# Performance work log

Hardware: AMD Instinct MI355X
Metric: run time of the kernel (lower is better)

## Reference

```python
import jax, jax.numpy as jnp
import numpy as np

B, S, HID = 1, 4096, 1024
HQ, HKV, D = 16, 4, 64   # query heads, kv heads (GQA), dim_per_head
ROPE_BASE = 10000.0


def setup_inputs() -> dict:
    key = jax.random.key(0)
    ks = jax.random.split(key, 5)
    s = 0.02
    return {
        "x": jax.random.normal(ks[0], (B, S, HID), jnp.float32),
        "Wq": jax.random.normal(ks[1], (HID, HQ * D), jnp.float32) * s,
        "Wk": jax.random.normal(ks[2], (HID, HKV * D), jnp.float32) * s,
        "Wv": jax.random.normal(ks[3], (HID, HKV * D), jnp.float32) * s,
        "Wo": jax.random.normal(ks[4], (HQ * D, HID), jnp.float32) * s,
    }


def _rope(t, cos, sin):
    # non-interleaved (half-split) rotary; t: [B,S,H,D], cos/sin: [S, D//2]
    t1, t2 = jnp.split(t, 2, axis=-1)
    c = cos[None, :, None, :]
    sn = sin[None, :, None, :]
    return jnp.concatenate([t1 * c - t2 * sn, t2 * c + t1 * sn], axis=-1)


def reference(x, Wq, Wk, Wv, Wo):
    # QKV projections (self-attention: key=value=query=x), reshape to [B,S,H,D]
    q = (x @ Wq).reshape(B, S, HQ, D)
    k = (x @ Wk).reshape(B, S, HKV, D)
    v = (x @ Wv).reshape(B, S, HKV, D)

    # rotary position embedding over full head dim
    inv_freq = 1.0 / (ROPE_BASE ** (jnp.arange(0, D, 2, dtype=jnp.float32) / D))
    ang = jnp.arange(S, dtype=jnp.float32)[:, None] * inv_freq[None, :]  # [S, D//2]
    cos, sin = jnp.cos(ang), jnp.sin(ang)
    q = _rope(q, cos, sin)
    k = _rope(k, cos, sin)

    # GQA: expand kv heads to match query heads
    g = HQ // HKV
    k = jnp.repeat(k, g, axis=2)
    v = jnp.repeat(v, g, axis=2)

    scale = D ** -0.5  # attn_scaling ** -0.5 with attn_scaling = dim_per_head
    scores = jnp.einsum('bqhd,bkhd->bhqk', q, k) * scale  # [B,HQ,S,S]
    causal = jnp.tril(jnp.ones((S, S), dtype=bool))
    scores = jnp.where(causal[None, None], scores, jnp.finfo(scores.dtype).min)
    attn = jax.nn.softmax(scores, axis=-1)

    ctx = jnp.einsum('bhqk,bkhd->bqhd', attn, v).reshape(B, S, HQ * D)
    return ctx @ Wo
```

## Files before the change

kernel.cpp:

```cpp
#include <hip/hip_runtime.h>
#include <hip/hip_bf16.h>
#include <math.h>

typedef __attribute__((ext_vector_type(8))) short short8;
typedef __attribute__((ext_vector_type(4))) float f32x4;

#define S_   4096
#define HQ_  16
#define HKV_ 4
#define D_   64

static __device__ __forceinline__ unsigned short f2b(float f) {
    __hip_bfloat16 h = __float2bfloat16(f);
    return *reinterpret_cast<unsigned short*>(&h);
}
static __device__ __forceinline__ float b2f(unsigned short u) {
    union { unsigned int u; float f; } c;
    c.u = ((unsigned int)u) << 16;
    return c.f;
}

typedef __attribute__((address_space(1))) const unsigned int gas_u32;
typedef __attribute__((address_space(3))) unsigned int las_u32;
static __device__ __forceinline__ void gload16(const void* g, void* l) {
    __builtin_amdgcn_global_load_lds((gas_u32*)g, (las_u32*)l, 16, 0, 0);
}


__global__ __launch_bounds__(256) void k_prep(const float* __restrict__ Wq,
                                              const float* __restrict__ Wk,
                                              const float* __restrict__ Wv,
                                              const float* __restrict__ Wo,
                                              const float* __restrict__ x,
                                              unsigned short* __restrict__ WT,
                                              unsigned short* __restrict__ WoT,
                                              unsigned short* __restrict__ xb,
                                              float* __restrict__ cs) {
    const int z = blockIdx.z;
    const int t = threadIdx.x;
    if (z == 4) {
        int flat = blockIdx.y * 32 + blockIdx.x;
#pragma unroll
        for (int ii = 0; ii < 4; ++ii) {
            int i = flat * 1024 + ii * 256 + t;
            float4 v = ((const float4*)x)[i];
            ushort4 o;
            o.x = f2b(v.x); o.y = f2b(v.y); o.z = f2b(v.z); o.w = f2b(v.w);
            ((ushort4*)xb)[i] = o;
        }
        return;
    }
    if (z == 5) {
        int flat = blockIdx.y * 32 + blockIdx.x;
        if (flat >= 512) return;
        int i = flat * 256 + t;
        int s = i >> 5, jj = i & 31;
        float invf = exp2f(-(float)jj * (13.287712379549449f / 32.0f));
        float ang = (float)s * invf;
        ((float2*)cs)[i] = make_float2(cosf(ang), sinf(ang));
        return;
    }
    const float* tin; unsigned short* tout; int N, gx;
    if (z == 0)      { tin = Wq; tout = WT;                 N = 1024; gx = 32; }
    else if (z == 1) { tin = Wk; tout = WT + 1024 * 1024;   N = 256;  gx = 8;  }
    else if (z == 2) { tin = Wv; tout = WT + 1280 * 1024;   N = 256;  gx = 8;  }
    else             { tin = Wo; tout = WoT;                N = 1024; gx = 32; }
    if ((int)blockIdx.x >= gx) return;
    __shared__ float tile[32][33];
    int tx = t & 31, ty = t >> 5;
    int n0 = blockIdx.x * 32, k0 = blockIdx.y * 32;
#pragma unroll
    for (int r = 0; r < 32; r += 8)
        tile[ty + r][tx] = tin[(size_t)(k0 + ty + r) * N + n0 + tx];
    __syncthreads();
#pragma unroll
    for (int r = 0; r < 32; r += 8)
        tout[(size_t)(n0 + ty + r) * 1024 + k0 + tx] = f2b(tile[tx][ty + r]);
}


__global__ __launch_bounds__(256) void k_gemm_qkv(const unsigned short* __restrict__ A,
                                                  const unsigned short* __restrict__ BT,
                                                  const float* __restrict__ cs,
                                                  unsigned short* __restrict__ Qr,
                                                  unsigned short* __restrict__ Kr,
                                                  unsigned short* __restrict__ Vt) {
    __shared__ unsigned short As[128 * 64];
    __shared__ unsigned short Bs[64 * 64];
    const int t = threadIdx.x;
    const int ntile = blockIdx.x;
    const int n0 = ntile * 64;
    const int m0 = blockIdx.y * 128;
    const int w = t >> 6, lane = t & 63, lr = lane & 15, lg = lane >> 4;
    const int sr = lane >> 3, sch = (lane & 7) * 16;
    const int K = 1024;

    f32x4 acc[2][4];
#pragma unroll
    for (int m = 0; m < 2; ++m)
#pragma unroll
        for (int n = 0; n < 4; ++n) acc[m][n] = (f32x4){0.f, 0.f, 0.f, 0.f};

    for (int k0 = 0; k0 < K; k0 += 64) {
#pragma unroll
        for (int c = 0; c < 4; ++c) {
            int r0 = w * 32 + c * 8;
            int r = r0 + sr;
            gload16((const char*)&A[(size_t)(m0 + r) * K + k0] + (sch ^ ((r & 7) << 4)),
                    (char*)As + r0 * 128);
        }
#pragma unroll
        for (int c = 0; c < 2; ++c) {
            int r0 = w * 16 + c * 8;
            int r = r0 + sr;
            gload16((const char*)&BT[(size_t)(n0 + r) * K + k0] + (sch ^ ((r & 7) << 4)),
                    (char*)Bs + r0 * 128);
        }
        __syncthreads();
#pragma unroll
        for (int kk = 0; kk < 2; ++kk) {
            short8 af[2], bf[4];
#pragma unroll
            for (int m = 0; m < 2; ++m) {
                int arow = w * 32 + m * 16 + lr;
                af[m] = *(const short8*)((const char*)As + arow * 128 +
                                         ((kk * 64 + lg * 16) ^ ((arow & 7) << 4)));
            }
#pragma unroll
            for (int n = 0; n < 4; ++n) {
                int brow = n * 16 + lr;
                bf[n] = *(const short8*)((const char*)Bs + brow * 128 +
                                         ((kk * 64 + lg * 16) ^ ((brow & 7) << 4)));
            }
#pragma unroll
            for (int m = 0; m < 2; ++m)
#pragma unroll
                for (int n = 0; n < 4; ++n)
                    acc[m][n] = __builtin_amdgcn_mfma_f32_16x16x32_bf16(af[m], bf[n], acc[m][n], 0, 0, 0);
        }
        __syncthreads();
    }

    if (ntile < 20) {
        const float QS = (ntile < 16) ? 0.125f * 1.44269504088896340736f : 1.0f;
        unsigned short* dst = (ntile < 16) ? (Qr + (size_t)ntile * (S_ * D_))
                                           : (Kr + (size_t)(ntile - 16) * (S_ * D_));
#pragma unroll
        for (int m = 0; m < 2; ++m)
#pragma unroll
            for (int rr = 0; rr < 4; ++rr) {
                int s = m0 + w * 32 + m * 16 + lg * 4 + rr;
                const float2* csr = (const float2*)cs + s * 32;
                float2 c0 = csr[lr];
                float2 c1 = csr[16 + lr];
                float t1 = acc[m][0][rr], t2 = acc[m][2][rr];
                dst[(size_t)s * 64 + lr]      = f2b((t1 * c0.x - t2 * c0.y) * QS);
                dst[(size_t)s * 64 + 32 + lr] = f2b((t2 * c0.x + t1 * c0.y) * QS);
                t1 = acc[m][1][rr]; t2 = acc[m][3][rr];
                dst[(size_t)s * 64 + 16 + lr] = f2b((t1 * c1.x - t2 * c1.y) * QS);
                dst[(size_t)s * 64 + 48 + lr] = f2b((t2 * c1.x + t1 * c1.y) * QS);
            }
    } else {
        int h2 = ntile - 20;
        unsigned short* dst = Vt + (size_t)h2 * (D_ * S_);
#pragma unroll
        for (int m = 0; m < 2; ++m)
#pragma unroll
            for (int n = 0; n < 4; ++n)
#pragma unroll
                for (int rr = 0; rr < 4; ++rr) {
                    int s = m0 + w * 32 + m * 16 + lg * 4 + rr;
                    dst[(size_t)(n * 16 + lr) * S_ + s] = f2b(acc[m][n][rr]);
                }
    }
}


__global__ __launch_bounds__(256) void k_gemm_o(const unsigned short* __restrict__ A,
                                                const unsigned short* __restrict__ BT,
                                                float* __restrict__ out) {
    __shared__ unsigned short As[128 * 64];
    __shared__ unsigned short Bs[64 * 64];
    const int t = threadIdx.x;
    const int n0 = blockIdx.x * 64;
    const int m0 = blockIdx.y * 128;
    const int w = t >> 6, lane = t & 63, lr = lane & 15, lg = lane >> 4;
    const int sr = lane >> 3, sch = (lane & 7) * 16;
    const int K = 1024;

    f32x4 acc[2][4];
#pragma unroll
    for (int m = 0; m < 2; ++m)
#pragma unroll
        for (int n = 0; n < 4; ++n) acc[m][n] = (f32x4){0.f, 0.f, 0.f, 0.f};

    for (int k0 = 0; k0 < K; k0 += 64) {
#pragma unroll
        for (int c = 0; c < 4; ++c) {
            int r0 = w * 32 + c * 8;
            int r = r0 + sr;
            gload16((const char*)&A[(size_t)(m0 + r) * K + k0] + (sch ^ ((r & 7) << 4)),
                    (char*)As + r0 * 128);
        }
#pragma unroll
        for (int c = 0; c < 2; ++c) {
            int r0 = w * 16 + c * 8;
            int r = r0 + sr;
            gload16((const char*)&BT[(size_t)(n0 + r) * K + k0] + (sch ^ ((r & 7) << 4)),
                    (char*)Bs + r0 * 128);
        }
        __syncthreads();
#pragma unroll
        for (int kk = 0; kk < 2; ++kk) {
            short8 af[2], bf[4];
#pragma unroll
            for (int m = 0; m < 2; ++m) {
                int arow = w * 32 + m * 16 + lr;
                af[m] = *(const short8*)((const char*)As + arow * 128 +
                                         ((kk * 64 + lg * 16) ^ ((arow & 7) << 4)));
            }
#pragma unroll
            for (int n = 0; n < 4; ++n) {
                int brow = n * 16 + lr;
                bf[n] = *(const short8*)((const char*)Bs + brow * 128 +
                                         ((kk * 64 + lg * 16) ^ ((brow & 7) << 4)));
            }
#pragma unroll
            for (int m = 0; m < 2; ++m)
#pragma unroll
                for (int n = 0; n < 4; ++n)
                    acc[m][n] = __builtin_amdgcn_mfma_f32_16x16x32_bf16(af[m], bf[n], acc[m][n], 0, 0, 0);
        }
        __syncthreads();
    }
#pragma unroll
    for (int m = 0; m < 2; ++m)
#pragma unroll
        for (int n = 0; n < 4; ++n)
#pragma unroll
            for (int rr = 0; rr < 4; ++rr) {
                int row = m0 + w * 32 + m * 16 + lg * 4 + rr;
                int col = n0 + n * 16 + lr;
                out[(size_t)row * 1024 + col] = acc[m][n][rr];
            }
}


__global__ __launch_bounds__(256, 2)
void k_attn(const unsigned short* __restrict__ Qr,
            const unsigned short* __restrict__ Kr,
            const unsigned short* __restrict__ Vt,
            unsigned short* __restrict__ Pacc,
            float* __restrict__ Psv) {
    __shared__ unsigned short Ks[2][64 * 64];
    __shared__ unsigned short Vs[2][64 * 64];
    __shared__ unsigned short Ps[4][32 * 64];

    const int t = threadIdx.x;
    const int p = blockIdx.x;
    const int h = blockIdx.y;
    const int j = blockIdx.z;
    const int kvh = h >> 2;
    const int w = t >> 6, lane = t & 63, lr = lane & 15, lg = lane >> 4;

    const unsigned short* Qh = Qr + (size_t)h * (S_ * D_);
    const unsigned short* Kh = Kr + (size_t)kvh * (S_ * D_);
    const unsigned short* Vh = Vt + (size_t)kvh * (D_ * S_);

    const int xw = (lr & 7) << 4;
    const int sr = lane >> 3, sch = (lane & 7) * 16;
    const int r0a = w * 16, r0b = w * 16 + 8;

#pragma unroll 1
    for (int half = 0; half < 2; ++half) {
        const int qb = half ? p : (31 - p);
        const int lastkb = 2 * qb + 1;
        const int qi0 = qb * 128 + w * 32 + lr;

        const char* kp[2];
        const char* vp[2];
        {
            int ra = r0a + sr, rb = r0b + sr;
            kp[0] = (const char*)(Kh + (size_t)(j * 64 + ra) * 64) + (sch ^ ((ra & 7) << 4));
            kp[1] = (const char*)(Kh + (size_t)(j * 64 + rb) * 64) + (sch ^ ((rb & 7) << 4));
            vp[0] = (const char*)(Vh + (size_t)ra * S_ + j * 64) + (sch ^ ((ra & 7) << 4));
            vp[1] = (const char*)(Vh + (size_t)rb * S_ + j * 64) + (sch ^ ((rb & 7) << 4));
        }
        auto stage = [&](int buf) {
            gload16(kp[0], (char*)&Ks[buf][0] + r0a * 128);
            gload16(kp[1], (char*)&Ks[buf][0] + r0b * 128);
            gload16(vp[0], (char*)&Vs[buf][0] + r0a * 128);
            gload16(vp[1], (char*)&Vs[buf][0] + r0b * 128);
            kp[0] += 16384; kp[1] += 16384;
            vp[0] += 256;   vp[1] += 256;
        };

        short8 aq[2][2];
        {
            int q0 = (qb * 128 + w * 32 + lr);
            aq[0][0] = *(const short8*)&Qh[(size_t)q0 * 64 + lg * 8];
            aq[0][1] = *(const short8*)&Qh[(size_t)q0 * 64 + 32 + lg * 8];
            aq[1][0] = *(const short8*)&Qh[(size_t)(q0 + 16) * 64 + lg * 8];
            aq[1][1] = *(const short8*)&Qh[(size_t)(q0 + 16) * 64 + 32 + lg * 8];
        }
        float svl0 = 0.f, svl1 = 0.f;
        f32x4 acc0[4], acc1[4];
#pragma unroll
        for (int i = 0; i < 4; ++i) { acc0[i] = (f32x4){0.f,0.f,0.f,0.f}; acc1[i] = (f32x4){0.f,0.f,0.f,0.f}; }

        int cur = 0;
        stage(0);
        __syncthreads();

        for (int kb = j; kb <= lastkb; kb += 2) {
            if (kb + 2 <= lastkb) stage(cur ^ 1);

            f32x4 s0[4], s1[4];
#pragma unroll
            for (int i = 0; i < 4; ++i) { s0[i] = (f32x4){0.f,0.f,0.f,0.f}; s1[i] = (f32x4){0.f,0.f,0.f,0.f}; }
            const char* KsB = (const char*)&Ks[cur][0];
            __builtin_amdgcn_s_setprio(1);
#pragma unroll
            for (int kk = 0; kk < 2; ++kk)
#pragma unroll
                for (int nt = 0; nt < 4; ++nt) {
                    int brow = nt * 16 + lr;
                    short8 kf = *(const short8*)(KsB + brow * 128 + ((kk * 64 + lg * 16) ^ xw));
                    s0[nt] = __builtin_amdgcn_mfma_f32_16x16x32_bf16(kf, aq[0][kk], s0[nt], 0, 0, 0);
                    s1[nt] = __builtin_amdgcn_mfma_f32_16x16x32_bf16(kf, aq[1][kk], s1[nt], 0, 0, 0);
                }
            __builtin_amdgcn_s_setprio(0);

            if (kb >= 2 * qb) {
                int kbase = kb * 64 + lg * 4;
#pragma unroll
                for (int nt = 0; nt < 4; ++nt)
#pragma unroll
                    for (int rr = 0; rr < 4; ++rr) {
                        int ki = kbase + nt * 16 + rr;
                        if (ki > qi0) s0[nt][rr] = -INFINITY;
                        if (ki > qi0 + 16) s1[nt][rr] = -INFINITY;
                    }
            }

            char* PwB = (char*)&Ps[w][0];
#pragma unroll
            for (int nt = 0; nt < 4; ++nt) {
                float p0 = exp2f(s0[nt][0]), p1 = exp2f(s0[nt][1]);
                float p2 = exp2f(s0[nt][2]), p3 = exp2f(s0[nt][3]);
                svl0 += (p0 + p1) + (p2 + p3);
                unsigned int w0, w1;
                asm("v_cvt_pk_bf16_f32 %0, %1, %2" : "=v"(w0) : "v"(p0), "v"(p1));
                asm("v_cvt_pk_bf16_f32 %0, %1, %2" : "=v"(w1) : "v"(p2), "v"(p3));
                union { unsigned int u32[2]; unsigned long long u64; } pk;
                pk.u32[0] = w0; pk.u32[1] = w1;
                *(unsigned long long*)(PwB + lr * 128 + ((nt * 32 + lg * 8) ^ xw)) = pk.u64;
            }
#pragma unroll
            for (int nt = 0; nt < 4; ++nt) {
                float p0 = exp2f(s1[nt][0]), p1 = exp2f(s1[nt][1]);
                float p2 = exp2f(s1[nt][2]), p3 = exp2f(s1[nt][3]);
                svl1 += (p0 + p1) + (p2 + p3);
                unsigned int w0, w1;
                asm("v_cvt_pk_bf16_f32 %0, %1, %2" : "=v"(w0) : "v"(p0), "v"(p1));
                asm("v_cvt_pk_bf16_f32 %0, %1, %2" : "=v"(w1) : "v"(p2), "v"(p3));
                union { unsigned int u32[2]; unsigned long long u64; } pk;
                pk.u32[0] = w0; pk.u32[1] = w1;
                *(unsigned long long*)(PwB + (16 + lr) * 128 + ((nt * 32 + lg * 8) ^ xw)) = pk.u64;
            }

            const char* VsB = (const char*)&Vs[cur][0];
            __builtin_amdgcn_s_setprio(1);
#pragma unroll
            for (int kk = 0; kk < 2; ++kk) {
                short8 pa0 = *(const short8*)(PwB + lr * 128 + ((kk * 64 + lg * 16) ^ xw));
                short8 pa1 = *(const short8*)(PwB + (16 + lr) * 128 + ((kk * 64 + lg * 16) ^ xw));
#pragma unroll
                for (int nt = 0; nt < 4; ++nt) {
                    int drow = nt * 16 + lr;
                    short8 vb = *(const short8*)(VsB + drow * 128 + ((kk * 64 + lg * 16) ^ xw));
                    acc0[nt] = __builtin_amdgcn_mfma_f32_16x16x32_bf16(pa0, vb, acc0[nt], 0, 0, 0);
                    acc1[nt] = __builtin_amdgcn_mfma_f32_16x16x32_bf16(pa1, vb, acc1[nt], 0, 0, 0);
                }
            }
            __builtin_amdgcn_s_setprio(0);

            __syncthreads();
            cur ^= 1;
        }

        svl0 += __shfl_xor(svl0, 16); svl0 += __shfl_xor(svl0, 32);
        svl1 += __shfl_xor(svl1, 16); svl1 += __shfl_xor(svl1, 32);
        const int u = (j * 32 + qb) * 16 + h;
        if (lg == 0) {
            Psv[u * 128 + w * 32 + lr] = svl0;
            Psv[u * 128 + w * 32 + 16 + lr] = svl1;
        }
        unsigned short* Pb = Pacc + (size_t)u * 8192;
#pragma unroll
        for (int nt = 0; nt < 4; ++nt)
#pragma unroll
            for (int rr = 0; rr < 4; ++rr) {
                int row0 = w * 32 + lg * 4 + rr;
                int col = nt * 16 + lr;
                Pb[row0 * 64 + col] = f2b(acc0[nt][rr]);
                Pb[(row0 + 16) * 64 + col] = f2b(acc1[nt][rr]);
            }
    }
}


__global__ __launch_bounds__(256) void k_combine(const unsigned short* __restrict__ Pacc,
                                                 const float* __restrict__ Psv,
                                                 unsigned short* __restrict__ O) {
    const int qb64 = blockIdx.x, h = blockIdx.y;
    const int t = threadIdx.x;
    const int r = t >> 2, db = (t & 3) * 16;
    const int qb128 = qb64 >> 1;
    const int rloc = (qb64 & 1) * 64 + r;
    const int u0 = qb128 * 16 + h;
    const int u1 = (32 + qb128) * 16 + h;
    float sa = Psv[u0 * 128 + rloc], sb = Psv[u1 * 128 + rloc];
    float inv = 1.f / (sa + sb);
    const unsigned short* A_ = Pacc + (size_t)u0 * 8192 + rloc * 64 + db;
    const unsigned short* B_ = Pacc + (size_t)u1 * 8192 + rloc * 64 + db;
    unsigned short* Op = O + (size_t)(qb64 * 64 + r) * 1024 + h * 64 + db;
#pragma unroll
    for (int halfv = 0; halfv < 2; ++halfv) {
        short8 va = *(const short8*)(A_ + halfv * 8);
        short8 vb = *(const short8*)(B_ + halfv * 8);
        short8 o;
#pragma unroll
        for (int i = 0; i < 8; ++i)
            o[i] = (short)f2b((b2f((unsigned short)va[i]) + b2f((unsigned short)vb[i])) * inv);
        *(short8*)(Op + halfv * 8) = o;
    }
}


extern "C" void kernel_launch(void* const* d_in, const int* in_sizes, int n_in,
                              void* d_out, int out_size, void* d_ws, size_t ws_size,
                              hipStream_t stream) {
    const float* x  = (const float*)d_in[0];
    const float* Wq = (const float*)d_in[1];
    const float* Wk = (const float*)d_in[2];
    const float* Wv = (const float*)d_in[3];
    const float* Wo = (const float*)d_in[4];
    float* out = (float*)d_out;
    char* ws = (char*)d_ws;

    unsigned short* WT  = (unsigned short*)(ws + 0);
    unsigned short* WoT = (unsigned short*)(ws + 3145728);
    unsigned short* Qr  = (unsigned short*)(ws + 5242880);
    unsigned short* Kr  = (unsigned short*)(ws + 13631488);
    unsigned short* Vt  = (unsigned short*)(ws + 15728640);
    unsigned short* O   = (unsigned short*)(ws + 17825792);
    float* cs           = (float*)(ws + 26214400);
    unsigned short* xb  = (unsigned short*)(ws + 27262976);
    unsigned short* Pacc = (unsigned short*)(ws + 27262976);
    float* Psv           = (float*)(ws + 44040192);

    k_prep<<<dim3(32, 32, 6), 256, 0, stream>>>(Wq, Wk, Wv, Wo, x, WT, WoT, xb, cs);
    k_gemm_qkv<<<dim3(24, 32), 256, 0, stream>>>(xb, WT, cs, Qr, Kr, Vt);
    k_attn<<<dim3(16, 16, 2), 256, 0, stream>>>(Qr, Kr, Vt, Pacc, Psv);
    k_combine<<<dim3(64, 16), 256, 0, stream>>>(Pacc, Psv, O);
    k_gemm_o<<<dim3(16, 32), 256, 0, stream>>>(O, WoT, out);
}
```

Measured before the change: 115.8 us.

## Halve attention query tile, keep P in registers, deepen GEMM K-step

The attention kernel now gives each wave 16 query rows (64-row blocks, twice as many blocks) and passes the softmax probabilities from the score MFMA output straight into the PV MFMA operand in registers. This removes the per-wave shared-memory P buffer and its write/read round trip. The V fragment load is split into two 8-byte loads to match the resulting register layout. Both GEMMs stage 128-wide K tiles per barrier instead of 64, with an occupancy hint of 3, which halves loop iterations and synchronisations at the cost of more LDS per block.

```diff
diff --git a/kernel.cpp b/kernel.cpp
--- a/kernel.cpp
+++ b/kernel.cpp
@@ -79,20 +79,22 @@
 }
 
 
-__global__ __launch_bounds__(256) void k_gemm_qkv(const unsigned short* __restrict__ A,
-                                                  const unsigned short* __restrict__ BT,
-                                                  const float* __restrict__ cs,
-                                                  unsigned short* __restrict__ Qr,
-                                                  unsigned short* __restrict__ Kr,
-                                                  unsigned short* __restrict__ Vt) {
-    __shared__ unsigned short As[128 * 64];
-    __shared__ unsigned short Bs[64 * 64];
+__global__ __launch_bounds__(256, 3)
+void k_gemm_qkv(const unsigned short* __restrict__ A,
+                const unsigned short* __restrict__ BT,
+                const float* __restrict__ cs,
+                unsigned short* __restrict__ Qr,
+                unsigned short* __restrict__ Kr,
+                unsigned short* __restrict__ Vt) {
+    __shared__ unsigned short As[128 * 128];
+    __shared__ unsigned short Bs[64 * 128];
     const int t = threadIdx.x;
     const int ntile = blockIdx.x;
     const int n0 = ntile * 64;
     const int m0 = blockIdx.y * 128;
     const int w = t >> 6, lane = t & 63, lr = lane & 15, lg = lane >> 4;
-    const int sr = lane >> 3, sch = (lane & 7) * 16;
+    const int srr = w * 4 + (lane >> 4);
+    const int sby = (lane & 15) * 16;
     const int K = 1024;
 
     f32x4 acc[2][4];
@@ -101,35 +103,33 @@
 #pragma unroll
         for (int n = 0; n < 4; ++n) acc[m][n] = (f32x4){0.f, 0.f, 0.f, 0.f};
 
-    for (int k0 = 0; k0 < K; k0 += 64) {
+    for (int k0 = 0; k0 < K; k0 += 128) {
+#pragma unroll
+        for (int c = 0; c < 8; ++c) {
+            int r = c * 16 + srr;
+            gload16((const char*)&A[(size_t)(m0 + r) * K + k0] + (sby ^ ((r & 7) << 4)),
+                    (char*)As + c * 4096 + w * 1024);
+        }
 #pragma unroll
         for (int c = 0; c < 4; ++c) {
-            int r0 = w * 32 + c * 8;
-            int r = r0 + sr;
-            gload16((const char*)&A[(size_t)(m0 + r) * K + k0] + (sch ^ ((r & 7) << 4)),
-                    (char*)As + r0 * 128);
-        }
-#pragma unroll
-        for (int c = 0; c < 2; ++c) {
-            int r0 = w * 16 + c * 8;
-            int r = r0 + sr;
-            gload16((const char*)&BT[(size_t)(n0 + r) * K + k0] + (sch ^ ((r & 7) << 4)),
-                    (char*)Bs + r0 * 128);
+            int r = c * 16 + srr;
+            gload16((const char*)&BT[(size_t)(n0 + r) * K + k0] + (sby ^ ((r & 7) << 4)),
+                    (char*)Bs + c * 4096 + w * 1024);
         }
         __syncthreads();
 #pragma unroll
-        for (int kk = 0; kk < 2; ++kk) {
+        for (int kk = 0; kk < 4; ++kk) {
             short8 af[2], bf[4];
 #pragma unroll
             for (int m = 0; m < 2; ++m) {
                 int arow = w * 32 + m * 16 + lr;
-                af[m] = *(const short8*)((const char*)As + arow * 128 +
+                af[m] = *(const short8*)((const char*)As + arow * 256 +
                                          ((kk * 64 + lg * 16) ^ ((arow & 7) << 4)));
             }
 #pragma unroll
             for (int n = 0; n < 4; ++n) {
                 int brow = n * 16 + lr;
-                bf[n] = *(const short8*)((const char*)Bs + brow * 128 +
+                bf[n] = *(const short8*)((const char*)Bs + brow * 256 +
                                          ((kk * 64 + lg * 16) ^ ((brow & 7) << 4)));
             }
 #pragma unroll
@@ -176,16 +176,18 @@
 }
 
 
-__global__ __launch_bounds__(256) void k_gemm_o(const unsigned short* __restrict__ A,
-                                                const unsigned short* __restrict__ BT,
-                                                float* __restrict__ out) {
-    __shared__ unsigned short As[128 * 64];
-    __shared__ unsigned short Bs[64 * 64];
+__global__ __launch_bounds__(256, 3)
+void k_gemm_o(const unsigned short* __restrict__ A,
+              const unsigned short* __restrict__ BT,
+              float* __restrict__ out) {
+    __shared__ unsigned short As[128 * 128];
+    __shared__ unsigned short Bs[64 * 128];
     const int t = threadIdx.x;
     const int n0 = blockIdx.x * 64;
     const int m0 = blockIdx.y * 128;
     const int w = t >> 6, lane = t & 63, lr = lane & 15, lg = lane >> 4;
-    const int sr = lane >> 3, sch = (lane & 7) * 16;
+    const int srr = w * 4 + (lane >> 4);
+    const int sby = (lane & 15) * 16;
     const int K = 1024;
 
     f32x4 acc[2][4];
@@ -194,35 +196,33 @@
 #pragma unroll
         for (int n = 0; n < 4; ++n) acc[m][n] = (f32x4){0.f, 0.f, 0.f, 0.f};
 
-    for (int k0 = 0; k0 < K; k0 += 64) {
+    for (int k0 = 0; k0 < K; k0 += 128) {
+#pragma unroll
+        for (int c = 0; c < 8; ++c) {
+            int r = c * 16 + srr;
+            gload16((const char*)&A[(size_t)(m0 + r) * K + k0] + (sby ^ ((r & 7) << 4)),
+                    (char*)As + c * 4096 + w * 1024);
+        }
 #pragma unroll
         for (int c = 0; c < 4; ++c) {
-            int r0 = w * 32 + c * 8;
-            int r = r0 + sr;
-            gload16((const char*)&A[(size_t)(m0 + r) * K + k0] + (sch ^ ((r & 7) << 4)),
-                    (char*)As + r0 * 128);
-        }
-#pragma unroll
-        for (int c = 0; c < 2; ++c) {
-            int r0 = w * 16 + c * 8;
-            int r = r0 + sr;
-            gload16((const char*)&BT[(size_t)(n0 + r) * K + k0] + (sch ^ ((r & 7) << 4)),
-                    (char*)Bs + r0 * 128);
+            int r = c * 16 + srr;
+            gload16((const char*)&BT[(size_t)(n0 + r) * K + k0] + (sby ^ ((r & 7) << 4)),
+                    (char*)Bs + c * 4096 + w * 1024);
         }
         __syncthreads();
 #pragma unroll
-        for (int kk = 0; kk < 2; ++kk) {
+        for (int kk = 0; kk < 4; ++kk) {
             short8 af[2], bf[4];
 #pragma unroll
             for (int m = 0; m < 2; ++m) {
                 int arow = w * 32 + m * 16 + lr;
-                af[m] = *(const short8*)((const char*)As + arow * 128 +
+                af[m] = *(const short8*)((const char*)As + arow * 256 +
                                          ((kk * 64 + lg * 16) ^ ((arow & 7) << 4)));
             }
 #pragma unroll
             for (int n = 0; n < 4; ++n) {
                 int brow = n * 16 + lr;
-                bf[n] = *(const short8*)((const char*)Bs + brow * 128 +
+                bf[n] = *(const short8*)((const char*)Bs + brow * 256 +
                                          ((kk * 64 + lg * 16) ^ ((brow & 7) << 4)));
             }
 #pragma unroll
@@ -246,7 +246,7 @@
 }
 
 
-__global__ __launch_bounds__(256, 2)
+__global__ __launch_bounds__(256, 4)
 void k_attn(const unsigned short* __restrict__ Qr,
             const unsigned short* __restrict__ Kr,
             const unsigned short* __restrict__ Vt,
@@ -254,7 +254,6 @@
             float* __restrict__ Psv) {
     __shared__ unsigned short Ks[2][64 * 64];
     __shared__ unsigned short Vs[2][64 * 64];
-    __shared__ unsigned short Ps[4][32 * 64];
 
     const int t = threadIdx.x;
     const int p = blockIdx.x;
@@ -273,9 +272,9 @@
 
 #pragma unroll 1
     for (int half = 0; half < 2; ++half) {
-        const int qb = half ? p : (31 - p);
-        const int lastkb = 2 * qb + 1;
-        const int qi0 = qb * 128 + w * 32 + lr;
+        const int qb = half ? p : (63 - p);
+        const int tend = qb + 1;
+        const int qi = qb * 64 + w * 16 + lr;
 
         const char* kp[2];
         const char* vp[2];
@@ -295,29 +294,27 @@
             vp[0] += 256;   vp[1] += 256;
         };
 
-        short8 aq[2][2];
+        short8 aq[2];
         {
-            int q0 = (qb * 128 + w * 32 + lr);
-            aq[0][0] = *(const short8*)&Qh[(size_t)q0 * 64 + lg * 8];
-            aq[0][1] = *(const short8*)&Qh[(size_t)q0 * 64 + 32 + lg * 8];
-            aq[1][0] = *(const short8*)&Qh[(size_t)(q0 + 16) * 64 + lg * 8];
-            aq[1][1] = *(const short8*)&Qh[(size_t)(q0 + 16) * 64 + 32 + lg * 8];
-        }
-        float svl0 = 0.f, svl1 = 0.f;
-        f32x4 acc0[4], acc1[4];
-#pragma unroll
-        for (int i = 0; i < 4; ++i) { acc0[i] = (f32x4){0.f,0.f,0.f,0.f}; acc1[i] = (f32x4){0.f,0.f,0.f,0.f}; }
+            int qrow = qb * 64 + w * 16 + lr;
+            aq[0] = *(const short8*)&Qh[(size_t)qrow * 64 + lg * 8];
+            aq[1] = *(const short8*)&Qh[(size_t)qrow * 64 + 32 + lg * 8];
+        }
+        float svl = 0.f;
+        f32x4 acc_o[4];
+#pragma unroll
+        for (int i = 0; i < 4; ++i) acc_o[i] = (f32x4){0.f, 0.f, 0.f, 0.f};
 
         int cur = 0;
         stage(0);
         __syncthreads();
 
-        for (int kb = j; kb <= lastkb; kb += 2) {
-            if (kb + 2 <= lastkb) stage(cur ^ 1);
-
-            f32x4 s0[4], s1[4];
-#pragma unroll
-            for (int i = 0; i < 4; ++i) { s0[i] = (f32x4){0.f,0.f,0.f,0.f}; s1[i] = (f32x4){0.f,0.f,0.f,0.f}; }
+        for (int kb = j; kb < tend; kb += 2) {
+            if (kb + 2 < tend) stage(cur ^ 1);
+
+            f32x4 s[4];
+#pragma unroll
+            for (int i = 0; i < 4; ++i) s[i] = (f32x4){0.f, 0.f, 0.f, 0.f};
             const char* KsB = (const char*)&Ks[cur][0];
             __builtin_amdgcn_s_setprio(1);
 #pragma unroll
@@ -326,61 +323,45 @@
                 for (int nt = 0; nt < 4; ++nt) {
                     int brow = nt * 16 + lr;
                     short8 kf = *(const short8*)(KsB + brow * 128 + ((kk * 64 + lg * 16) ^ xw));
-                    s0[nt] = __builtin_amdgcn_mfma_f32_16x16x32_bf16(kf, aq[0][kk], s0[nt], 0, 0, 0);
-                    s1[nt] = __builtin_amdgcn_mfma_f32_16x16x32_bf16(kf, aq[1][kk], s1[nt], 0, 0, 0);
+                    s[nt] = __builtin_amdgcn_mfma_f32_16x16x32_bf16(kf, aq[kk], s[nt], 0, 0, 0);
                 }
             __builtin_amdgcn_s_setprio(0);
 
-            if (kb >= 2 * qb) {
+            if (kb == qb) {
                 int kbase = kb * 64 + lg * 4;
 #pragma unroll
                 for (int nt = 0; nt < 4; ++nt)
 #pragma unroll
-                    for (int rr = 0; rr < 4; ++rr) {
-                        int ki = kbase + nt * 16 + rr;
-                        if (ki > qi0) s0[nt][rr] = -INFINITY;
-                        if (ki > qi0 + 16) s1[nt][rr] = -INFINITY;
-                    }
-            }
-
-            char* PwB = (char*)&Ps[w][0];
+                    for (int rr = 0; rr < 4; ++rr)
+                        if (kbase + nt * 16 + rr > qi) s[nt][rr] = -INFINITY;
+            }
+
+            unsigned int wd[8];
 #pragma unroll
             for (int nt = 0; nt < 4; ++nt) {
-                float p0 = exp2f(s0[nt][0]), p1 = exp2f(s0[nt][1]);
-                float p2 = exp2f(s0[nt][2]), p3 = exp2f(s0[nt][3]);
-                svl0 += (p0 + p1) + (p2 + p3);
-                unsigned int w0, w1;
-                asm("v_cvt_pk_bf16_f32 %0, %1, %2" : "=v"(w0) : "v"(p0), "v"(p1));
-                asm("v_cvt_pk_bf16_f32 %0, %1, %2" : "=v"(w1) : "v"(p2), "v"(p3));
-                union { unsigned int u32[2]; unsigned long long u64; } pk;
-                pk.u32[0] = w0; pk.u32[1] = w1;
-                *(unsigned long long*)(PwB + lr * 128 + ((nt * 32 + lg * 8) ^ xw)) = pk.u64;
-            }
-#pragma unroll
-            for (int nt = 0; nt < 4; ++nt) {
-                float p0 = exp2f(s1[nt][0]), p1 = exp2f(s1[nt][1]);
-                float p2 = exp2f(s1[nt][2]), p3 = exp2f(s1[nt][3]);
-                svl1 += (p0 + p1) + (p2 + p3);
-                unsigned int w0, w1;
-                asm("v_cvt_pk_bf16_f32 %0, %1, %2" : "=v"(w0) : "v"(p0), "v"(p1));
-                asm("v_cvt_pk_bf16_f32 %0, %1, %2" : "=v"(w1) : "v"(p2), "v"(p3));
-                union { unsigned int u32[2]; unsigned long long u64; } pk;
-                pk.u32[0] = w0; pk.u32[1] = w1;
-                *(unsigned long long*)(PwB + (16 + lr) * 128 + ((nt * 32 + lg * 8) ^ xw)) = pk.u64;
+                float p0 = exp2f(s[nt][0]), p1 = exp2f(s[nt][1]);
+                float p2 = exp2f(s[nt][2]), p3 = exp2f(s[nt][3]);
+                svl += (p0 + p1) + (p2 + p3);
+                asm("v_cvt_pk_bf16_f32 %0, %1, %2" : "=v"(wd[nt * 2])     : "v"(p0), "v"(p1));
+                asm("v_cvt_pk_bf16_f32 %0, %1, %2" : "=v"(wd[nt * 2 + 1]) : "v"(p2), "v"(p3));
             }
 
             const char* VsB = (const char*)&Vs[cur][0];
             __builtin_amdgcn_s_setprio(1);
 #pragma unroll
             for (int kk = 0; kk < 2; ++kk) {
-                short8 pa0 = *(const short8*)(PwB + lr * 128 + ((kk * 64 + lg * 16) ^ xw));
-                short8 pa1 = *(const short8*)(PwB + (16 + lr) * 128 + ((kk * 64 + lg * 16) ^ xw));
+                union { unsigned int u[4]; short8 s8; } pa;
+                pa.u[0] = wd[4 * kk + 0]; pa.u[1] = wd[4 * kk + 1];
+                pa.u[2] = wd[4 * kk + 2]; pa.u[3] = wd[4 * kk + 3];
 #pragma unroll
                 for (int nt = 0; nt < 4; ++nt) {
                     int drow = nt * 16 + lr;
-                    short8 vb = *(const short8*)(VsB + drow * 128 + ((kk * 64 + lg * 16) ^ xw));
-                    acc0[nt] = __builtin_amdgcn_mfma_f32_16x16x32_bf16(pa0, vb, acc0[nt], 0, 0, 0);
-                    acc1[nt] = __builtin_amdgcn_mfma_f32_16x16x32_bf16(pa1, vb, acc1[nt], 0, 0, 0);
+                    union { unsigned long long q[2]; short8 s8; } vb;
+                    vb.q[0] = *(const unsigned long long*)(VsB + drow * 128 +
+                              ((kk * 64 + lg * 8) ^ xw));
+                    vb.q[1] = *(const unsigned long long*)(VsB + drow * 128 +
+                              ((kk * 64 + 32 + lg * 8) ^ xw));
+                    acc_o[nt] = __builtin_amdgcn_mfma_f32_16x16x32_bf16(pa.s8, vb.s8, acc_o[nt], 0, 0, 0);
                 }
             }
             __builtin_amdgcn_s_setprio(0);
@@ -389,23 +370,20 @@
             cur ^= 1;
         }
 
-        svl0 += __shfl_xor(svl0, 16); svl0 += __shfl_xor(svl0, 32);
-        svl1 += __shfl_xor(svl1, 16); svl1 += __shfl_xor(svl1, 32);
-        const int u = (j * 32 + qb) * 16 + h;
-        if (lg == 0) {
-            Psv[u * 128 + w * 32 + lr] = svl0;
-            Psv[u * 128 + w * 32 + 16 + lr] = svl1;
-        }
-        unsigned short* Pb = Pacc + (size_t)u * 8192;
-#pragma unroll
-        for (int nt = 0; nt < 4; ++nt)
-#pragma unroll
-            for (int rr = 0; rr < 4; ++rr) {
-                int row0 = w * 32 + lg * 4 + rr;
-                int col = nt * 16 + lr;
-                Pb[row0 * 64 + col] = f2b(acc0[nt][rr]);
-                Pb[(row0 + 16) * 64 + col] = f2b(acc1[nt][rr]);
-            }
+        svl += __shfl_xor(svl, 16);
+        svl += __shfl_xor(svl, 32);
+        const int u = ((j * 64 + qb) * 16 + h);
+        if (lg == 0) Psv[u * 64 + w * 16 + lr] = svl;
+        unsigned short* Pb = Pacc + (size_t)u * 4096;
+#pragma unroll
+        for (int nt = 0; nt < 4; ++nt) {
+            int rr = w * 16 + lg * 4;
+            int col = nt * 16 + lr;
+            Pb[(rr + 0) * 64 + col] = f2b(acc_o[nt][0]);
+            Pb[(rr + 1) * 64 + col] = f2b(acc_o[nt][1]);
+            Pb[(rr + 2) * 64 + col] = f2b(acc_o[nt][2]);
+            Pb[(rr + 3) * 64 + col] = f2b(acc_o[nt][3]);
+        }
     }
 }
 
@@ -413,18 +391,16 @@
 __global__ __launch_bounds__(256) void k_combine(const unsigned short* __restrict__ Pacc,
                                                  const float* __restrict__ Psv,
                                                  unsigned short* __restrict__ O) {
-    const int qb64 = blockIdx.x, h = blockIdx.y;
+    const int qb = blockIdx.x, h = blockIdx.y;
     const int t = threadIdx.x;
     const int r = t >> 2, db = (t & 3) * 16;
-    const int qb128 = qb64 >> 1;
-    const int rloc = (qb64 & 1) * 64 + r;
-    const int u0 = qb128 * 16 + h;
-    const int u1 = (32 + qb128) * 16 + h;
-    float sa = Psv[u0 * 128 + rloc], sb = Psv[u1 * 128 + rloc];
+    const int u0 = (qb * 16 + h);
+    const int u1 = ((64 + qb) * 16 + h);
+    float sa = Psv[u0 * 64 + r], sb = Psv[u1 * 64 + r];
     float inv = 1.f / (sa + sb);
-    const unsigned short* A_ = Pacc + (size_t)u0 * 8192 + rloc * 64 + db;
-    const unsigned short* B_ = Pacc + (size_t)u1 * 8192 + rloc * 64 + db;
-    unsigned short* Op = O + (size_t)(qb64 * 64 + r) * 1024 + h * 64 + db;
+    const unsigned short* A_ = Pacc + (size_t)u0 * 4096 + r * 64 + db;
+    const unsigned short* B_ = Pacc + (size_t)u1 * 4096 + r * 64 + db;
+    unsigned short* Op = O + (size_t)(qb * 64 + r) * 1024 + h * 64 + db;
 #pragma unroll
     for (int halfv = 0; halfv < 2; ++halfv) {
         short8 va = *(const short8*)(A_ + halfv * 8);
@@ -462,7 +438,7 @@
 
     k_prep<<<dim3(32, 32, 6), 256, 0, stream>>>(Wq, Wk, Wv, Wo, x, WT, WoT, xb, cs);
     k_gemm_qkv<<<dim3(24, 32), 256, 0, stream>>>(xb, WT, cs, Qr, Kr, Vt);
-    k_attn<<<dim3(16, 16, 2), 256, 0, stream>>>(Qr, Kr, Vt, Pacc, Psv);
+    k_attn<<<dim3(32, 16, 2), 256, 0, stream>>>(Qr, Kr, Vt, Pacc, Psv);
     k_combine<<<dim3(64, 16), 256, 0, stream>>>(Pacc, Psv, O);
     k_gemm_o<<<dim3(16, 32), 256, 0, stream>>>(O, WoT, out);
 }
```

Measured after the change: 120.6 us. 1.04x slower.
